# Kernel optimization log

Hardware: AMD Instinct MI355X
Metric: run time of the kernel (lower is better)

## Reference

```python
import jax, jax.numpy as jnp
import numpy as np
import math

B, N, HW, D, H = 4, 1024, 4096, 512, 8
DK = D // H
EPS = 0.1


def setup_inputs() -> dict:
    key = jax.random.key(0)
    ks = jax.random.split(key, 12)
    s = 1.0 / math.sqrt(D)
    query = jax.random.normal(ks[0], (B, N, D), dtype=jnp.float32)
    key_t = jax.random.normal(ks[1], (B, HW, D), dtype=jnp.float32)
    value = jax.random.normal(ks[2], (B, HW, D), dtype=jnp.float32)
    # 2D spatial positions of the feature map in [0,1]^2
    x_tilde = jax.random.uniform(ks[3], (HW, 2), dtype=jnp.float32)
    # predicted positions per query: close to x_tilde so each row has unmasked keys
    x_hat = x_tilde[None, :, :] + 0.1 * jax.random.normal(ks[4], (N, HW, 2), dtype=jnp.float32)
    Wq = jax.random.normal(ks[5], (D, D), dtype=jnp.float32) * s
    Wk = jax.random.normal(ks[6], (D, D), dtype=jnp.float32) * s
    Wv = jax.random.normal(ks[7], (D, D), dtype=jnp.float32) * s
    Wo = jax.random.normal(ks[8], (D, D), dtype=jnp.float32) * s
    bq = jnp.zeros((D,), jnp.float32)
    bk = jnp.zeros((D,), jnp.float32)
    bv = jnp.zeros((D,), jnp.float32)
    bo = jnp.zeros((D,), jnp.float32)
    return {"query": query, "key": key_t, "value": value,
            "x_tilde": x_tilde, "x_hat": x_hat,
            "Wq": Wq, "bq": bq, "Wk": Wk, "bk": bk,
            "Wv": Wv, "bv": bv, "Wo": Wo, "bo": bo}


def reference(query, key, value, x_tilde, x_hat, Wq, bq, Wk, bk, Wv, bv, Wo, bo):
    b, n, d = query.shape
    hw = key.shape[1]
    # nn.Linear: x @ W^T + b
    Q = (query @ Wq.T + bq).reshape(b, n, H, DK).transpose(0, 2, 1, 3)   # [B,H,N,DK]
    K = (key @ Wk.T + bk).reshape(b, hw, H, DK).transpose(0, 2, 1, 3)    # [B,H,HW,DK]
    V = (value @ Wv.T + bv).reshape(b, hw, H, DK).transpose(0, 2, 1, 3)  # [B,H,HW,DK]
    scores = jnp.einsum('bhnd,bhmd->bhnm', Q, K) / math.sqrt(DK)         # [B,H,N,HW]
    # geometric mask: 0 where ||x_tilde_j - x_hat_ij|| < eps else -inf
    dist = jnp.linalg.norm(x_tilde[None, :, :] - x_hat, axis=-1)         # [N,HW]
    m_geo = jnp.where(dist < EPS, 0.0, -jnp.inf).astype(scores.dtype)
    scores = scores + m_geo[None, None, :, :]
    attn = jax.nn.softmax(scores, axis=-1)                               # [B,H,N,HW]
    # dropout is identity in eval mode
    ctx = jnp.einsum('bhnm,bhmd->bhnd', attn, V)                         # [B,H,N,DK]
    ctx = ctx.transpose(0, 2, 1, 3).reshape(b, n, d)
    out = ctx @ Wo.T + bo
    return (out, attn)
```

## Files before the change

kernel.cpp:

```cpp
#include <hip/hip_runtime.h>
#include <math.h>

typedef _Float16 h8 __attribute__((ext_vector_type(8)));
typedef _Float16 h4 __attribute__((ext_vector_type(4)));
typedef float    f4 __attribute__((ext_vector_type(4)));

#define NQ    1024
#define HWK   4096
#define DM    512
#define NH    8
#define DKH   64

__device__ inline h8 cvt_h8(const float* __restrict__ p) {
    const f4* q = (const f4*)p;
    f4 a = q[0], b = q[1];
    h8 r;
    r[0] = (_Float16)a[0]; r[1] = (_Float16)a[1];
    r[2] = (_Float16)a[2]; r[3] = (_Float16)a[3];
    r[4] = (_Float16)b[0]; r[5] = (_Float16)b[1];
    r[6] = (_Float16)b[2]; r[7] = (_Float16)b[3];
    return r;
}

__global__ __launch_bounds__(256)
void mask_kernel(const float* __restrict__ x_tilde, const float* __restrict__ x_hat,
                 _Float16* __restrict__ maskT)
{
    __shared__ _Float16 T[64][72];
    int t  = threadIdx.x;
    int jl = t & 63;
    int iw = t >> 6;
    int j0 = blockIdx.x * 64;
    int i0 = blockIdx.y * 64;

    float xt0 = x_tilde[(j0 + jl) * 2 + 0];
    float xt1 = x_tilde[(j0 + jl) * 2 + 1];

    for (int ii = iw; ii < 64; ii += 4) {
        size_t idx = ((size_t)(i0 + ii) * HWK + j0 + jl) * 2;
        float h0 = x_hat[idx + 0];
        float h1 = x_hat[idx + 1];
        float dx = xt0 - h0, dy = xt1 - h1;
        float d2 = __fadd_rn(__fmul_rn(dx, dx), __fmul_rn(dy, dy));
        float dist = __fsqrt_rn(d2);
        T[ii][jl] = (dist < 0.1f) ? (_Float16)0.0f : (_Float16)(-__builtin_inff());
    }
    __syncthreads();
    int il = t & 63;
    for (int jj = iw; jj < 64; jj += 4) {
        maskT[(size_t)(j0 + jj) * NQ + i0 + il] = T[il][jj];
    }
}

__global__ __launch_bounds__(256)
void proj_qk(const float* __restrict__ X, const float* __restrict__ W,
             const float* __restrict__ bias, _Float16* __restrict__ out,
             int nlog2, float scale)
{
    int tid = threadIdx.x;
    int w = tid >> 6, lane = tid & 63, q = lane >> 4, c = lane & 15;
    int wr = blockIdx.x * 128 + (w >> 1) * 64;
    int wc = blockIdx.y * 128 + (w & 1) * 64;

    f4 acc[4][4];
    const f4 fz = {0.f, 0.f, 0.f, 0.f};
#pragma unroll
    for (int i = 0; i < 4; i++)
#pragma unroll
        for (int j = 0; j < 4; j++) acc[i][j] = fz;

    for (int k0 = 0; k0 < DM; k0 += 32) {
        h8 af[4], bf[4];
#pragma unroll
        for (int i = 0; i < 4; i++)
            af[i] = cvt_h8(X + (size_t)(wr + i * 16 + c) * DM + k0 + q * 8);
#pragma unroll
        for (int j = 0; j < 4; j++)
            bf[j] = cvt_h8(W + (size_t)(wc + j * 16 + c) * DM + k0 + q * 8);
#pragma unroll
        for (int i = 0; i < 4; i++)
#pragma unroll
            for (int j = 0; j < 4; j++)
                acc[i][j] = __builtin_amdgcn_mfma_f32_16x16x32_f16(af[i], bf[j], acc[i][j], 0, 0, 0);
    }

    int nmask = (1 << nlog2) - 1;
#pragma unroll
    for (int j = 0; j < 4; j++) {
        int ncol = wc + j * 16 + c;
        float bb = bias[ncol];
        int hh = ncol >> 6, dk = ncol & 63;
#pragma unroll
        for (int i = 0; i < 4; i++) {
#pragma unroll
            for (int r = 0; r < 4; r++) {
                int m = wr + i * 16 + q * 4 + r;
                int b = m >> nlog2, n = m & nmask;
                float v = (acc[i][j][r] + bb) * scale;
                out[((((size_t)(b * NH + hh)) << nlog2) + n) * DKH + dk] = (_Float16)v;
            }
        }
    }
}

__global__ __launch_bounds__(256)
void proj_v(const float* __restrict__ V, const float* __restrict__ W,
            const float* __restrict__ bias, _Float16* __restrict__ out)
{
    int tid = threadIdx.x;
    int w = tid >> 6, lane = tid & 63, q = lane >> 4, c = lane & 15;
    int wr = blockIdx.x * 128 + (w >> 1) * 64;
    int wc = blockIdx.y * 128 + (w & 1) * 64;

    f4 acc[4][4];
    const f4 fz = {0.f, 0.f, 0.f, 0.f};
#pragma unroll
    for (int i = 0; i < 4; i++)
#pragma unroll
        for (int j = 0; j < 4; j++) acc[i][j] = fz;

    for (int k0 = 0; k0 < DM; k0 += 32) {
        h8 af[4], bf[4];
#pragma unroll
        for (int i = 0; i < 4; i++)
            af[i] = cvt_h8(W + (size_t)(wr + i * 16 + c) * DM + k0 + q * 8);
#pragma unroll
        for (int j = 0; j < 4; j++)
            bf[j] = cvt_h8(V + (size_t)(wc + j * 16 + c) * DM + k0 + q * 8);
#pragma unroll
        for (int i = 0; i < 4; i++)
#pragma unroll
            for (int j = 0; j < 4; j++)
                acc[i][j] = __builtin_amdgcn_mfma_f32_16x16x32_f16(af[i], bf[j], acc[i][j], 0, 0, 0);
    }

#pragma unroll
    for (int i = 0; i < 4; i++) {
#pragma unroll
        for (int r = 0; r < 4; r++) {
            int f = wr + i * 16 + q * 4 + r;
            float bb = bias[f];
            int hh = f >> 6, dk = f & 63;
#pragma unroll
            for (int j = 0; j < 4; j++) {
                int col = wc + j * 16 + c;
                int b = col >> 12, hw = col & 4095;
                out[((size_t)(b * NH + hh) * DKH + dk) * HWK + hw] =
                    (_Float16)(acc[i][j][r] + bb);
            }
        }
    }
}

__global__ __launch_bounds__(256)
void proj_o(const _Float16* __restrict__ C, const float* __restrict__ W,
            const float* __restrict__ bias, float* __restrict__ out)
{
    int tid = threadIdx.x;
    int w = tid >> 6, lane = tid & 63, q = lane >> 4, c = lane & 15;
    int wr = blockIdx.x * 128 + (w >> 1) * 64;
    int wc = blockIdx.y * 128 + (w & 1) * 64;

    f4 acc[4][4];
    const f4 fz = {0.f, 0.f, 0.f, 0.f};
#pragma unroll
    for (int i = 0; i < 4; i++)
#pragma unroll
        for (int j = 0; j < 4; j++) acc[i][j] = fz;

    for (int k0 = 0; k0 < DM; k0 += 32) {
        h8 af[4], bf[4];
#pragma unroll
        for (int i = 0; i < 4; i++)
            af[i] = *(const h8*)(C + (size_t)(wr + i * 16 + c) * DM + k0 + q * 8);
#pragma unroll
        for (int j = 0; j < 4; j++)
            bf[j] = cvt_h8(W + (size_t)(wc + j * 16 + c) * DM + k0 + q * 8);
#pragma unroll
        for (int i = 0; i < 4; i++)
#pragma unroll
            for (int j = 0; j < 4; j++)
                acc[i][j] = __builtin_amdgcn_mfma_f32_16x16x32_f16(af[i], bf[j], acc[i][j], 0, 0, 0);
    }

#pragma unroll
    for (int j = 0; j < 4; j++) {
        int ncol = wc + j * 16 + c;
        float bb = bias[ncol];
#pragma unroll
        for (int i = 0; i < 4; i++) {
#pragma unroll
            for (int r = 0; r < 4; r++) {
                int m = wr + i * 16 + q * 4 + r;
                out[(size_t)m * DM + ncol] = acc[i][j][r] + bb;
            }
        }
    }
}

__global__ __launch_bounds__(256)
void attn_kernel(const _Float16* __restrict__ Qh, const _Float16* __restrict__ Kh,
                 const _Float16* __restrict__ Vt, const _Float16* __restrict__ maskT,
                 float* __restrict__ attn_out, _Float16* __restrict__ ctx_h)
{
    __shared__ union SmU {
        _Float16 P[4][64][72];
        float    C[64][68];
    } sm;
    __shared__ float red[4][64];
    __shared__ float invl[64];

    int tid = threadIdx.x;
    int w = tid >> 6, lane = tid & 63, q = lane >> 4, c = lane & 15;
    int bh = blockIdx.x >> 4;
    int n0 = (blockIdx.x & 15) * 64;
    int b = bh >> 3, h = bh & 7;

    const _Float16* Qb = Qh + ((size_t)bh * NQ + n0) * DKH;
    const _Float16* Kb = Kh + (size_t)bh * HWK * DKH;
    const _Float16* Vb = Vt + (size_t)bh * DKH * HWK;
    float* attn_b = attn_out + ((size_t)bh * NQ + n0) * HWK;

    h8 qa[4][2];
#pragma unroll
    for (int i = 0; i < 4; i++)
#pragma unroll
        for (int ks = 0; ks < 2; ks++)
            qa[i][ks] = *(const h8*)(Qb + (size_t)(i * 16 + c) * DKH + ks * 32 + q * 8);

    float lsum[4][4];
#pragma unroll
    for (int i = 0; i < 4; i++)
#pragma unroll
        for (int r = 0; r < 4; r++) lsum[i][r] = 0.f;

    for (int it = 0; it < 16; ++it) {
        int m0 = it * 256 + w * 64;
        h8 kb[4][2];
#pragma unroll
        for (int j = 0; j < 4; j++)
#pragma unroll
            for (int ks = 0; ks < 2; ks++)
                kb[j][ks] = *(const h8*)(Kb + (size_t)(m0 + j * 16 + c) * DKH + ks * 32 + q * 8);
#pragma unroll
        for (int i = 0; i < 4; i++) {
#pragma unroll
            for (int j = 0; j < 4; j++) {
                f4 acc = {0.f, 0.f, 0.f, 0.f};
                acc = __builtin_amdgcn_mfma_f32_16x16x32_f16(qa[i][0], kb[j][0], acc, 0, 0, 0);
                acc = __builtin_amdgcn_mfma_f32_16x16x32_f16(qa[i][1], kb[j][1], acc, 0, 0, 0);
                h4 mk = *(const h4*)(maskT + (size_t)(m0 + j * 16 + c) * NQ + n0 + i * 16 + q * 4);
#pragma unroll
                for (int r = 0; r < 4; r++)
                    lsum[i][r] += __expf(acc[r] + (float)mk[r]);
            }
        }
    }

#pragma unroll
    for (int i = 0; i < 4; i++) {
#pragma unroll
        for (int r = 0; r < 4; r++) {
            float s = lsum[i][r];
            s += __shfl_xor(s, 1);
            s += __shfl_xor(s, 2);
            s += __shfl_xor(s, 4);
            s += __shfl_xor(s, 8);
            if (c == 0) red[w][i * 16 + q * 4 + r] = s;
        }
    }
    __syncthreads();
    if (tid < 64)
        invl[tid] = 1.0f / (red[0][tid] + red[1][tid] + red[2][tid] + red[3][tid]);
    __syncthreads();

    f4 cacc[4][4];
    const f4 fz = {0.f, 0.f, 0.f, 0.f};
#pragma unroll
    for (int i = 0; i < 4; i++)
#pragma unroll
        for (int jd = 0; jd < 4; jd++) cacc[i][jd] = fz;

    for (int it = 0; it < 16; ++it) {
        int m0 = it * 256 + w * 64;
        h8 kb[4][2];
#pragma unroll
        for (int j = 0; j < 4; j++)
#pragma unroll
            for (int ks = 0; ks < 2; ks++)
                kb[j][ks] = *(const h8*)(Kb + (size_t)(m0 + j * 16 + c) * DKH + ks * 32 + q * 8);

#pragma unroll
        for (int i = 0; i < 4; i++) {
#pragma unroll
            for (int j = 0; j < 4; j++) {
                f4 acc = {0.f, 0.f, 0.f, 0.f};
                acc = __builtin_amdgcn_mfma_f32_16x16x32_f16(qa[i][0], kb[j][0], acc, 0, 0, 0);
                acc = __builtin_amdgcn_mfma_f32_16x16x32_f16(qa[i][1], kb[j][1], acc, 0, 0, 0);
                h4 mk = *(const h4*)(maskT + (size_t)(m0 + j * 16 + c) * NQ + n0 + i * 16 + q * 4);
#pragma unroll
                for (int r = 0; r < 4; r++) {
                    float e = __expf(acc[r] + (float)mk[r]);
                    sm.P[w][i * 16 + q * 4 + r][j * 16 + c] = (_Float16)e;
                }
            }
        }
#pragma unroll
        for (int ks = 0; ks < 2; ks++) {
            h8 pa[4], vb[4];
#pragma unroll
            for (int i = 0; i < 4; i++)
                pa[i] = *(const h8*)&sm.P[w][i * 16 + c][ks * 32 + q * 8];
#pragma unroll
            for (int jd = 0; jd < 4; jd++)
                vb[jd] = *(const h8*)(Vb + (size_t)(jd * 16 + c) * HWK + m0 + ks * 32 + q * 8);
#pragma unroll
            for (int i = 0; i < 4; i++)
#pragma unroll
                for (int jd = 0; jd < 4; jd++)
                    cacc[i][jd] = __builtin_amdgcn_mfma_f32_16x16x32_f16(pa[i], vb[jd], cacc[i][jd], 0, 0, 0);
        }
#pragma unroll
        for (int r0 = 0; r0 < 64; r0 += 4) {
            int row = r0 + q;
            h4 pv = *(const h4*)&sm.P[w][row][c * 4];
            float il = invl[row];
            f4 o;
            o[0] = (float)pv[0] * il;
            o[1] = (float)pv[1] * il;
            o[2] = (float)pv[2] * il;
            o[3] = (float)pv[3] * il;
            *(f4*)(attn_b + (size_t)row * HWK + m0 + c * 4) = o;
        }
    }

    __syncthreads();
    for (int idx = tid; idx < 64 * 68; idx += 256)
        (&sm.C[0][0])[idx] = 0.f;
    __syncthreads();
#pragma unroll
    for (int i = 0; i < 4; i++)
#pragma unroll
        for (int jd = 0; jd < 4; jd++)
#pragma unroll
            for (int r = 0; r < 4; r++)
                atomicAdd(&sm.C[i * 16 + q * 4 + r][jd * 16 + c], cacc[i][jd][r]);
    __syncthreads();

    _Float16* ctx_b = ctx_h + ((size_t)b * NQ + n0) * DM + h * DKH;
    for (int r0 = 0; r0 < 64; r0 += 4) {
        int row = r0 + w;
        int col = tid & 63;
        float v = sm.C[row][col] * invl[row];
        ctx_b[(size_t)row * DM + col] = (_Float16)v;
    }
}

extern "C" void kernel_launch(void* const* d_in, const int* in_sizes, int n_in,
                              void* d_out, int out_size, void* d_ws, size_t ws_size,
                              hipStream_t stream)
{
    const float* query   = (const float*)d_in[0];
    const float* key     = (const float*)d_in[1];
    const float* value   = (const float*)d_in[2];
    const float* x_tilde = (const float*)d_in[3];
    const float* x_hat   = (const float*)d_in[4];
    const float* Wq = (const float*)d_in[5];
    const float* bq = (const float*)d_in[6];
    const float* Wk = (const float*)d_in[7];
    const float* bk = (const float*)d_in[8];
    const float* Wv = (const float*)d_in[9];
    const float* bv = (const float*)d_in[10];
    const float* Wo = (const float*)d_in[11];
    const float* bo = (const float*)d_in[12];

    char* ws = (char*)d_ws;
    _Float16* Qh    = (_Float16*)(ws);
    _Float16* Kh    = (_Float16*)(ws + ((size_t)4  << 20));
    _Float16* Vt    = (_Float16*)(ws + ((size_t)20 << 20));
    _Float16* ctxh  = (_Float16*)(ws + ((size_t)36 << 20));
    _Float16* maskT = (_Float16*)(ws + ((size_t)40 << 20));

    float* out  = (float*)d_out;
    float* attn = out + (size_t)4 * NQ * DM;

    mask_kernel<<<dim3(HWK / 64, NQ / 64), 256, 0, stream>>>(x_tilde, x_hat, maskT);
    proj_qk<<<dim3(4 * NQ / 128, DM / 128), 256, 0, stream>>>(query, Wq, bq, Qh, 10, 0.125f);
    proj_qk<<<dim3(4 * HWK / 128, DM / 128), 256, 0, stream>>>(key, Wk, bk, Kh, 12, 1.0f);
    proj_v<<<dim3(DM / 128, 4 * HWK / 128), 256, 0, stream>>>(value, Wv, bv, Vt);
    attn_kernel<<<32 * (NQ / 64), 256, 0, stream>>>(Qh, Kh, Vt, maskT, attn, ctxh);
    proj_o<<<dim3(4 * NQ / 128, DM / 128), 256, 0, stream>>>(ctxh, Wo, bo, out);
}
```

Baseline: 1.032 ms.

## Pre-convert projection inputs and weights to fp16, add nontemporal loads/stores

Adds a standalone fp32→fp16 conversion kernel that runs over query, key, value and the four weight matrices before the projection GEMMs. The GEMMs then read fp16 directly, halving the bytes each one loads and dropping per-tile conversion work, since each input tile is re-read by several blocks. Large streaming accesses are also marked nontemporal: the x_hat loads, the attn output stores and the final output stores. The cost is seven extra kernel launches plus one extra full read and write pass over the inputs (about 40MB).

```diff
diff --git a/kernel.cpp b/kernel.cpp
--- a/kernel.cpp
+++ b/kernel.cpp
@@ -11,15 +11,20 @@
 #define NH    8
 #define DKH   64
 
-__device__ inline h8 cvt_h8(const float* __restrict__ p) {
-    const f4* q = (const f4*)p;
-    f4 a = q[0], b = q[1];
+__global__ __launch_bounds__(256)
+void cvt_f16_kernel(const float* __restrict__ in, _Float16* __restrict__ out, int n8)
+{
+    int i = blockIdx.x * blockDim.x + threadIdx.x;
+    if (i >= n8) return;
+    const f4* q = (const f4*)(in + (size_t)i * 8);
+    f4 a = __builtin_nontemporal_load(q);
+    f4 b = __builtin_nontemporal_load(q + 1);
     h8 r;
     r[0] = (_Float16)a[0]; r[1] = (_Float16)a[1];
     r[2] = (_Float16)a[2]; r[3] = (_Float16)a[3];
     r[4] = (_Float16)b[0]; r[5] = (_Float16)b[1];
     r[6] = (_Float16)b[2]; r[7] = (_Float16)b[3];
-    return r;
+    *(h8*)(out + (size_t)i * 8) = r;
 }
 
 __global__ __launch_bounds__(256)
@@ -38,8 +43,8 @@
 
     for (int ii = iw; ii < 64; ii += 4) {
         size_t idx = ((size_t)(i0 + ii) * HWK + j0 + jl) * 2;
-        float h0 = x_hat[idx + 0];
-        float h1 = x_hat[idx + 1];
+        float h0 = __builtin_nontemporal_load(x_hat + idx + 0);
+        float h1 = __builtin_nontemporal_load(x_hat + idx + 1);
         float dx = xt0 - h0, dy = xt1 - h1;
         float d2 = __fadd_rn(__fmul_rn(dx, dx), __fmul_rn(dy, dy));
         float dist = __fsqrt_rn(d2);
@@ -53,7 +58,7 @@
 }
 
 __global__ __launch_bounds__(256)
-void proj_qk(const float* __restrict__ X, const float* __restrict__ W,
+void proj_qk(const _Float16* __restrict__ X, const _Float16* __restrict__ W,
              const float* __restrict__ bias, _Float16* __restrict__ out,
              int nlog2, float scale)
 {
@@ -73,10 +78,10 @@
         h8 af[4], bf[4];
 #pragma unroll
         for (int i = 0; i < 4; i++)
-            af[i] = cvt_h8(X + (size_t)(wr + i * 16 + c) * DM + k0 + q * 8);
+            af[i] = *(const h8*)(X + (size_t)(wr + i * 16 + c) * DM + k0 + q * 8);
 #pragma unroll
         for (int j = 0; j < 4; j++)
-            bf[j] = cvt_h8(W + (size_t)(wc + j * 16 + c) * DM + k0 + q * 8);
+            bf[j] = *(const h8*)(W + (size_t)(wc + j * 16 + c) * DM + k0 + q * 8);
 #pragma unroll
         for (int i = 0; i < 4; i++)
 #pragma unroll
@@ -104,7 +109,7 @@
 }
 
 __global__ __launch_bounds__(256)
-void proj_v(const float* __restrict__ V, const float* __restrict__ W,
+void proj_v(const _Float16* __restrict__ V, const _Float16* __restrict__ W,
             const float* __restrict__ bias, _Float16* __restrict__ out)
 {
     int tid = threadIdx.x;
@@ -123,10 +128,10 @@
         h8 af[4], bf[4];
 #pragma unroll
         for (int i = 0; i < 4; i++)
-            af[i] = cvt_h8(W + (size_t)(wr + i * 16 + c) * DM + k0 + q * 8);
+            af[i] = *(const h8*)(W + (size_t)(wr + i * 16 + c) * DM + k0 + q * 8);
 #pragma unroll
         for (int j = 0; j < 4; j++)
-            bf[j] = cvt_h8(V + (size_t)(wc + j * 16 + c) * DM + k0 + q * 8);
+            bf[j] = *(const h8*)(V + (size_t)(wc + j * 16 + c) * DM + k0 + q * 8);
 #pragma unroll
         for (int i = 0; i < 4; i++)
 #pragma unroll
@@ -153,7 +158,7 @@
 }
 
 __global__ __launch_bounds__(256)
-void proj_o(const _Float16* __restrict__ C, const float* __restrict__ W,
+void proj_o(const _Float16* __restrict__ C, const _Float16* __restrict__ W,
             const float* __restrict__ bias, float* __restrict__ out)
 {
     int tid = threadIdx.x;
@@ -175,7 +180,7 @@
             af[i] = *(const h8*)(C + (size_t)(wr + i * 16 + c) * DM + k0 + q * 8);
 #pragma unroll
         for (int j = 0; j < 4; j++)
-            bf[j] = cvt_h8(W + (size_t)(wc + j * 16 + c) * DM + k0 + q * 8);
+            bf[j] = *(const h8*)(W + (size_t)(wc + j * 16 + c) * DM + k0 + q * 8);
 #pragma unroll
         for (int i = 0; i < 4; i++)
 #pragma unroll
@@ -192,7 +197,7 @@
 #pragma unroll
             for (int r = 0; r < 4; r++) {
                 int m = wr + i * 16 + q * 4 + r;
-                out[(size_t)m * DM + ncol] = acc[i][j][r] + bb;
+                __builtin_nontemporal_store(acc[i][j][r] + bb, &out[(size_t)m * DM + ncol]);
             }
         }
     }
@@ -330,7 +335,7 @@
             o[1] = (float)pv[1] * il;
             o[2] = (float)pv[2] * il;
             o[3] = (float)pv[3] * il;
-            *(f4*)(attn_b + (size_t)row * HWK + m0 + c * 4) = o;
+            __builtin_nontemporal_store(o, (f4*)(attn_b + (size_t)row * HWK + m0 + c * 4));
         }
     }
 
@@ -380,14 +385,30 @@
     _Float16* Vt    = (_Float16*)(ws + ((size_t)20 << 20));
     _Float16* ctxh  = (_Float16*)(ws + ((size_t)36 << 20));
     _Float16* maskT = (_Float16*)(ws + ((size_t)40 << 20));
+    _Float16* Xq    = (_Float16*)(ws + ((size_t)48 << 20));
+    _Float16* Xk    = (_Float16*)(ws + ((size_t)52 << 20));
+    _Float16* Xv    = (_Float16*)(ws + ((size_t)68 << 20));
+    _Float16* Wqh   = (_Float16*)(ws + ((size_t)84 << 20));
+    _Float16* Wkh   = (_Float16*)(ws + ((size_t)84 << 20) + (512 * 1024));
+    _Float16* Wvh   = (_Float16*)(ws + ((size_t)84 << 20) + (1024 * 1024));
+    _Float16* Woh   = (_Float16*)(ws + ((size_t)84 << 20) + (1536 * 1024));
 
     float* out  = (float*)d_out;
     float* attn = out + (size_t)4 * NQ * DM;
 
+    const int NW8 = DM * DM / 8;
+    cvt_f16_kernel<<<(4 * NQ * DM / 8 + 255) / 256, 256, 0, stream>>>(query, Xq, 4 * NQ * DM / 8);
+    cvt_f16_kernel<<<(4 * HWK * DM / 8 + 255) / 256, 256, 0, stream>>>(key, Xk, 4 * HWK * DM / 8);
+    cvt_f16_kernel<<<(4 * HWK * DM / 8 + 255) / 256, 256, 0, stream>>>(value, Xv, 4 * HWK * DM / 8);
+    cvt_f16_kernel<<<(NW8 + 255) / 256, 256, 0, stream>>>(Wq, Wqh, NW8);
+    cvt_f16_kernel<<<(NW8 + 255) / 256, 256, 0, stream>>>(Wk, Wkh, NW8);
+    cvt_f16_kernel<<<(NW8 + 255) / 256, 256, 0, stream>>>(Wv, Wvh, NW8);
+    cvt_f16_kernel<<<(NW8 + 255) / 256, 256, 0, stream>>>(Wo, Woh, NW8);
+
     mask_kernel<<<dim3(HWK / 64, NQ / 64), 256, 0, stream>>>(x_tilde, x_hat, maskT);
-    proj_qk<<<dim3(4 * NQ / 128, DM / 128), 256, 0, stream>>>(query, Wq, bq, Qh, 10, 0.125f);
-    proj_qk<<<dim3(4 * HWK / 128, DM / 128), 256, 0, stream>>>(key, Wk, bk, Kh, 12, 1.0f);
-    proj_v<<<dim3(DM / 128, 4 * HWK / 128), 256, 0, stream>>>(value, Wv, bv, Vt);
+    proj_qk<<<dim3(4 * NQ / 128, DM / 128), 256, 0, stream>>>(Xq, Wqh, bq, Qh, 10, 0.125f);
+    proj_qk<<<dim3(4 * HWK / 128, DM / 128), 256, 0, stream>>>(Xk, Wkh, bk, Kh, 12, 1.0f);
+    proj_v<<<dim3(DM / 128, 4 * HWK / 128), 256, 0, stream>>>(Xv, Wvh, bv, Vt);
     attn_kernel<<<32 * (NQ / 64), 256, 0, stream>>>(Qh, Kh, Vt, maskT, attn, ctxh);
-    proj_o<<<dim3(4 * NQ / 128, DM / 128), 256, 0, stream>>>(ctxh, Wo, bo, out);
-}
+    proj_o<<<dim3(4 * NQ / 128, DM / 128), 256, 0, stream>>>(ctxh, Woh, bo, out);
+}
```

Result: faster. 953.1 us (-7.7%).
